# Kernel tuning notes

Hardware: AMD Instinct MI355X
Metric: run time of the kernel (lower is better)

## Reference

```python
import jax, jax.numpy as jnp
import numpy as np

IN, OUT, N = 4096, 4096, 8192

def setup_inputs() -> dict:
    key = jax.random.key(0)
    k = jax.random.split(key, 7)
    sigma_start = 1.0  # log_sigma init = log(1.0) = 0; we use small randn instead for generality
    return {
        "x": jax.random.normal(k[0], (N, IN), dtype=jnp.float32),
        "mu_weight": jax.random.normal(k[1], (OUT, IN), dtype=jnp.float32) * 0.02,
        "log_sigma_weight": jax.random.normal(k[2], (OUT, IN), dtype=jnp.float32) * 0.1 - 3.0,
        "mu_bias": jax.random.normal(k[3], (OUT,), dtype=jnp.float32) * 0.02,
        "log_sigma_bias": jax.random.normal(k[4], (OUT,), dtype=jnp.float32) * 0.1 - 3.0,
        "eps_w": jax.random.normal(k[5], (OUT, IN), dtype=jnp.float32),
        "eps_b": jax.random.normal(k[6], (OUT,), dtype=jnp.float32),
    }

def reference(x, mu_weight, log_sigma_weight, mu_bias, log_sigma_bias, eps_w, eps_b):
    # Reparameterized Gaussian weight sampling: W = mu + exp(log_sigma) * eps
    weight = mu_weight + jnp.exp(log_sigma_weight) * eps_w        # [OUT, IN]
    bias = mu_bias + jnp.exp(log_sigma_bias) * eps_b              # [OUT]
    # F.linear(x, W, b) = x @ W^T + b
    return jnp.einsum("ni,oi->no", x, weight) + bias               # [N, OUT]
```

## Files before the change

### kernel.cpp

```cpp
#include <hip/hip_runtime.h>
#include <hip/hip_bf16.h>
#include <stdint.h>


constexpr int M    = 8192;
constexpr int K    = 4096;
constexpr int NOUT = 4096;

typedef __bf16 bf16x8 __attribute__((ext_vector_type(8)));
typedef float  f32x4  __attribute__((ext_vector_type(4)));
typedef short  short8 __attribute__((ext_vector_type(8)));

#define DI __device__ __forceinline__

DI void gl_lds16(const void* g, void* l) {
  __builtin_amdgcn_global_load_lds(
      (__attribute__((address_space(1))) void*)(g),
      (__attribute__((address_space(3))) void*)(l),
      16, 0, 0);
}

union BF8 {
  __hip_bfloat16 h[8];
  short8 s;
};

__global__ __launch_bounds__(256) void cast_x_kernel(const float* __restrict__ x,
                                                     short* __restrict__ xb) {
  int i = blockIdx.x * 256 + threadIdx.x;
  const float4* src = (const float4*)x;
  float4 f0 = src[2 * i + 0];
  float4 f1 = src[2 * i + 1];
  BF8 u;
  u.h[0] = __float2bfloat16(f0.x);
  u.h[1] = __float2bfloat16(f0.y);
  u.h[2] = __float2bfloat16(f0.z);
  u.h[3] = __float2bfloat16(f0.w);
  u.h[4] = __float2bfloat16(f1.x);
  u.h[5] = __float2bfloat16(f1.y);
  u.h[6] = __float2bfloat16(f1.z);
  u.h[7] = __float2bfloat16(f1.w);
  ((short8*)xb)[i] = u.s;
}

__global__ __launch_bounds__(256) void w_fuse_kernel(const float* __restrict__ mu,
                                                     const float* __restrict__ ls,
                                                     const float* __restrict__ eps,
                                                     short* __restrict__ wb) {
  int i = blockIdx.x * 256 + threadIdx.x;
  const float4* mu4 = (const float4*)mu;
  const float4* ls4 = (const float4*)ls;
  const float4* ep4 = (const float4*)eps;
  float4 m0 = mu4[2 * i + 0], m1 = mu4[2 * i + 1];
  float4 l0 = ls4[2 * i + 0], l1 = ls4[2 * i + 1];
  float4 e0 = ep4[2 * i + 0], e1 = ep4[2 * i + 1];
  BF8 u;
  u.h[0] = __float2bfloat16(m0.x + __expf(l0.x) * e0.x);
  u.h[1] = __float2bfloat16(m0.y + __expf(l0.y) * e0.y);
  u.h[2] = __float2bfloat16(m0.z + __expf(l0.z) * e0.z);
  u.h[3] = __float2bfloat16(m0.w + __expf(l0.w) * e0.w);
  u.h[4] = __float2bfloat16(m1.x + __expf(l1.x) * e1.x);
  u.h[5] = __float2bfloat16(m1.y + __expf(l1.y) * e1.y);
  u.h[6] = __float2bfloat16(m1.z + __expf(l1.z) * e1.z);
  u.h[7] = __float2bfloat16(m1.w + __expf(l1.w) * e1.w);
  ((short8*)wb)[i] = u.s;
}

__global__ __launch_bounds__(256) void bias_kernel(const float* __restrict__ mu_b,
                                                   const float* __restrict__ ls_b,
                                                   const float* __restrict__ eps_b,
                                                   float* __restrict__ bias) {
  int i = blockIdx.x * 256 + threadIdx.x;
  if (i < NOUT) bias[i] = mu_b[i] + expf(ls_b[i]) * eps_b[i];
}

__global__ __launch_bounds__(256) void gemm_bt_kernel(const short* __restrict__ A,
                                                      const short* __restrict__ B,
                                                      const float* __restrict__ bias,
                                                      float* __restrict__ C) {
  constexpr int BM = 128, BN = 128, BK = 32;
  __shared__ short As[BM * BK];
  __shared__ short Bs[BN * BK];

  const int tid  = threadIdx.x;
  const int lane = tid & 63;
  const int wave = tid >> 6;
  const int wm   = wave >> 1;
  const int wn   = wave & 1;
  const int m0   = blockIdx.y * BM;
  const int n0   = blockIdx.x * BN;
  const int mrow = lane & 15;
  const int quad = lane >> 4;

  f32x4 acc[4][4] = {};

  for (int k0 = 0; k0 < K; k0 += BK) {
#pragma unroll
    for (int it = 0; it < 2; ++it) {
      int cb  = it * 256 + wave * 64;
      int c   = cb + lane;
      int row = c >> 2;
      int q   = c & 3;
      gl_lds16(A + (size_t)(m0 + row) * K + k0 + q * 8, (char*)As + cb * 16);
      gl_lds16(B + (size_t)(n0 + row) * K + k0 + q * 8, (char*)Bs + cb * 16);
    }
    __syncthreads();

    bf16x8 a[4], b[4];
#pragma unroll
    for (int mi = 0; mi < 4; ++mi)
      a[mi] = *(const bf16x8*)&As[(wm * 64 + mi * 16 + mrow) * BK + quad * 8];
#pragma unroll
    for (int ni = 0; ni < 4; ++ni)
      b[ni] = *(const bf16x8*)&Bs[(wn * 64 + ni * 16 + mrow) * BK + quad * 8];

#pragma unroll
    for (int mi = 0; mi < 4; ++mi)
#pragma unroll
      for (int ni = 0; ni < 4; ++ni)
        acc[mi][ni] = __builtin_amdgcn_mfma_f32_16x16x32_bf16(a[mi], b[ni], acc[mi][ni], 0, 0, 0);

    __syncthreads();
  }

#pragma unroll
  for (int ni = 0; ni < 4; ++ni) {
    int col  = n0 + wn * 64 + ni * 16 + mrow;
    float bv = bias[col];
#pragma unroll
    for (int mi = 0; mi < 4; ++mi) {
      int rowb = m0 + wm * 64 + mi * 16 + quad * 4;
#pragma unroll
      for (int r = 0; r < 4; ++r)
        C[(size_t)(rowb + r) * NOUT + col] = acc[mi][ni][r] + bv;
    }
  }
}

extern "C" void kernel_launch(void* const* d_in, const int* in_sizes, int n_in,
                              void* d_out, int out_size, void* d_ws, size_t ws_size,
                              hipStream_t stream) {
  const float* x    = (const float*)d_in[0];
  const float* mu_w = (const float*)d_in[1];
  const float* ls_w = (const float*)d_in[2];
  const float* mu_b = (const float*)d_in[3];
  const float* ls_b = (const float*)d_in[4];
  const float* ep_w = (const float*)d_in[5];
  const float* ep_b = (const float*)d_in[6];
  float* out = (float*)d_out;

  char* ws = (char*)d_ws;
  short* xb   = (short*)(ws);
  short* wb   = (short*)(ws + (size_t)M * K * 2);
  float* bias = (float*)(ws + (size_t)M * K * 2 + (size_t)NOUT * K * 2);

  cast_x_kernel<<<(M * (size_t)K) / 8 / 256, 256, 0, stream>>>(x, xb);
  w_fuse_kernel<<<((size_t)NOUT * K) / 8 / 256, 256, 0, stream>>>(mu_w, ls_w, ep_w, wb);
  bias_kernel<<<(NOUT + 255) / 256, 256, 0, stream>>>(mu_b, ls_b, ep_b, bias);

  dim3 grid(NOUT / 128, M / 128);
  gemm_bt_kernel<<<grid, 256, 0, stream>>>(xb, wb, bias, out);
}
```

Measured before the change: 679.3 us.

## Rewrite GEMM with 256x256 tiles, 4-stage LDS pipeline, swizzle and XCD block remap

Grows the GEMM tile to 256x256 with 512 threads (8 waves, each computing 128x64). It adds a four-buffer LDS ring filled three stages ahead with direct global-to-LDS loads, and uses vmcnt waits plus a single barrier per iteration in place of two syncthreads. It also XOR-swizzles the LDS slots to cut bank conflicts, remaps block IDs so neighbouring tiles land on the same XCD for L2 reuse, and raises MFMA priority with setprio. The aim is to hide global load latency and raise arithmetic intensity, at the cost of 128 KB of LDS and more accumulator registers, which may limit occupancy.

```diff
diff --git a/kernel.cpp b/kernel.cpp
--- a/kernel.cpp
+++ b/kernel.cpp
@@ -74,62 +74,105 @@
   if (i < NOUT) bias[i] = mu_b[i] + expf(ls_b[i]) * eps_b[i];
 }
 
-__global__ __launch_bounds__(256) void gemm_bt_kernel(const short* __restrict__ A,
-                                                      const short* __restrict__ B,
-                                                      const float* __restrict__ bias,
-                                                      float* __restrict__ C) {
-  constexpr int BM = 128, BN = 128, BK = 32;
-  __shared__ short As[BM * BK];
-  __shared__ short Bs[BN * BK];
+constexpr int BM = 256, BN = 256, BK = 32;
+constexpr int NT = K / BK;
+
+__global__ __launch_bounds__(512, 2) void gemm_bt_kernel(const short* __restrict__ A,
+                                                         const short* __restrict__ B,
+                                                         const float* __restrict__ bias,
+                                                         float* __restrict__ C) {
+  __shared__ __align__(16) short Alds[4][BM * BK];
+  __shared__ __align__(16) short Blds[4][BN * BK];
 
   const int tid  = threadIdx.x;
   const int lane = tid & 63;
   const int wave = tid >> 6;
-  const int wm   = wave >> 1;
-  const int wn   = wave & 1;
-  const int m0   = blockIdx.y * BM;
-  const int n0   = blockIdx.x * BN;
+  const int wm   = wave >> 2;
+  const int wn   = wave & 3;
   const int mrow = lane & 15;
   const int quad = lane >> 4;
 
-  f32x4 acc[4][4] = {};
-
-  for (int k0 = 0; k0 < K; k0 += BK) {
-#pragma unroll
-    for (int it = 0; it < 2; ++it) {
-      int cb  = it * 256 + wave * 64;
-      int c   = cb + lane;
-      int row = c >> 2;
-      int q   = c & 3;
-      gl_lds16(A + (size_t)(m0 + row) * K + k0 + q * 8, (char*)As + cb * 16);
-      gl_lds16(B + (size_t)(n0 + row) * K + k0 + q * 8, (char*)Bs + cb * 16);
-    }
-    __syncthreads();
-
-    bf16x8 a[4], b[4];
-#pragma unroll
-    for (int mi = 0; mi < 4; ++mi)
-      a[mi] = *(const bf16x8*)&As[(wm * 64 + mi * 16 + mrow) * BK + quad * 8];
-#pragma unroll
-    for (int ni = 0; ni < 4; ++ni)
-      b[ni] = *(const bf16x8*)&Bs[(wn * 64 + ni * 16 + mrow) * BK + quad * 8];
-
-#pragma unroll
-    for (int mi = 0; mi < 4; ++mi)
-#pragma unroll
-      for (int ni = 0; ni < 4; ++ni)
-        acc[mi][ni] = __builtin_amdgcn_mfma_f32_16x16x32_bf16(a[mi], b[ni], acc[mi][ni], 0, 0, 0);
-
-    __syncthreads();
+  const int bid = blockIdx.x;
+  const int swz = (bid & 7) * 64 + (bid >> 3);
+  const int m0  = (swz >> 4) * BM;
+  const int n0  = (swz & 15) * BN;
+
+  const int c0 = tid, c1 = 512 + tid;
+  const int cb0 = (wave << 6);
+  const int cb1 = 512 + (wave << 6);
+  const int r0 = c0 >> 2, r1 = c1 >> 2;
+  const int sl0 = (c0 & 3) ^ ((r0 >> 1) & 3);
+  const int sl1 = (c1 & 3) ^ ((r1 >> 1) & 3);
+  const short* gA0 = A + (size_t)(m0 + r0) * K + sl0 * 8;
+  const short* gA1 = A + (size_t)(m0 + r1) * K + sl1 * 8;
+  const short* gB0 = B + (size_t)(n0 + r0) * K + sl0 * 8;
+  const short* gB1 = B + (size_t)(n0 + r1) * K + sl1 * 8;
+
+  const int slot = quad ^ ((mrow >> 1) & 3);
+  const int aOff = (wm * 128 + mrow) * 64 + slot * 16;
+  const int bOff = (wn * 64 + mrow) * 64 + slot * 16;
+
+  f32x4 acc[8][4] = {};
+
+#define STAGE(tt)                                           \
+  do {                                                      \
+    const int _b = (tt) & 3;                                \
+    const int _k = (tt) * BK;                               \
+    gl_lds16(gA0 + _k, (char*)Alds[_b] + cb0 * 16);         \
+    gl_lds16(gA1 + _k, (char*)Alds[_b] + cb1 * 16);         \
+    gl_lds16(gB0 + _k, (char*)Blds[_b] + cb0 * 16);         \
+    gl_lds16(gB1 + _k, (char*)Blds[_b] + cb1 * 16);         \
+  } while (0)
+
+#define COMPUTE(tt)                                                              \
+  do {                                                                           \
+    const char* _Ab = (const char*)Alds[(tt) & 3] + aOff;                        \
+    const char* _Bb = (const char*)Blds[(tt) & 3] + bOff;                        \
+    bf16x8 a[8], b[4];                                                           \
+    _Pragma("unroll") for (int mi = 0; mi < 8; ++mi)                             \
+        a[mi] = *(const bf16x8*)(_Ab + mi * 1024);                               \
+    _Pragma("unroll") for (int ni = 0; ni < 4; ++ni)                             \
+        b[ni] = *(const bf16x8*)(_Bb + ni * 1024);                               \
+    __builtin_amdgcn_s_setprio(1);                                               \
+    _Pragma("unroll") for (int mi = 0; mi < 8; ++mi)                             \
+        _Pragma("unroll") for (int ni = 0; ni < 4; ++ni)                         \
+            acc[mi][ni] =                                                        \
+                __builtin_amdgcn_mfma_f32_16x16x32_bf16(a[mi], b[ni],            \
+                                                        acc[mi][ni], 0, 0, 0);  \
+    __builtin_amdgcn_s_setprio(0);                                               \
+  } while (0)
+
+  STAGE(0);
+  STAGE(1);
+  STAGE(2);
+  asm volatile("s_waitcnt vmcnt(8)" ::: "memory");
+  __builtin_amdgcn_s_barrier();
+
+#pragma unroll 4
+  for (int t = 0; t < NT - 3; ++t) {
+    STAGE(t + 3);
+    COMPUTE(t);
+    asm volatile("s_waitcnt vmcnt(8)" ::: "memory");
+    __builtin_amdgcn_s_barrier();
   }
+  COMPUTE(NT - 3);
+  asm volatile("s_waitcnt vmcnt(4)" ::: "memory");
+  __builtin_amdgcn_s_barrier();
+  COMPUTE(NT - 2);
+  asm volatile("s_waitcnt vmcnt(0)" ::: "memory");
+  __builtin_amdgcn_s_barrier();
+  COMPUTE(NT - 1);
+
+#undef STAGE
+#undef COMPUTE
 
 #pragma unroll
   for (int ni = 0; ni < 4; ++ni) {
-    int col  = n0 + wn * 64 + ni * 16 + mrow;
-    float bv = bias[col];
+    const int col  = n0 + wn * 64 + ni * 16 + mrow;
+    const float bv = bias[col];
 #pragma unroll
-    for (int mi = 0; mi < 4; ++mi) {
-      int rowb = m0 + wm * 64 + mi * 16 + quad * 4;
+    for (int mi = 0; mi < 8; ++mi) {
+      const int rowb = m0 + wm * 128 + mi * 16 + quad * 4;
 #pragma unroll
       for (int r = 0; r < 4; ++r)
         C[(size_t)(rowb + r) * NOUT + col] = acc[mi][ni][r] + bv;
@@ -158,6 +201,5 @@
   w_fuse_kernel<<<((size_t)NOUT * K) / 8 / 256, 256, 0, stream>>>(mu_w, ls_w, ep_w, wb);
   bias_kernel<<<(NOUT + 255) / 256, 256, 0, stream>>>(mu_b, ls_b, ep_b, bias);
 
-  dim3 grid(NOUT / 128, M / 128);
-  gemm_bt_kernel<<<grid, 256, 0, stream>>>(xb, wb, bias, out);
-}
+  gemm_bt_kernel<<<(M / BM) * (NOUT / BN), 512, 0, stream>>>(xb, wb, bias, out);
+}
```

Result: faster. 625.0 us (-8.0%).
